# Optimization experiments

Measured on AMD Instinct MI355X. Metric: run time of the kernel, lower is better.

The kernel has to match this reference:

```python
import jax, jax.numpy as jnp
import numpy as np
from jax import lax


def _conv1d(z, w):
    # z: [B, C_in, L], w: [C_out, C_in, K], stride 1, padding 1 -> [B, C_out, L]
    return lax.conv_general_dilated(
        z, w, window_strides=(1,), padding=[(1, 1)],
        dimension_numbers=("NCH", "OIH", "NCH"))


def setup_inputs() -> dict:
    key = jax.random.key(0)
    k1, k2, k3 = jax.random.split(key, 3)
    B, T, C, H, L, K = 16, 64, 128, 256, 128, 3
    x = jax.random.normal(k1, (B, T, C, L), dtype=jnp.float32)
    # small init so tanh stays in its useful range
    W_i = jax.random.normal(k2, (H, C, K), dtype=jnp.float32) * 0.05
    W_h = jax.random.normal(k3, (H, H, K), dtype=jnp.float32) * 0.05
    return {"x": x, "W_i": W_i, "W_h": W_h}


def reference(x, W_i, W_h):
    # Conv1DRnn, single layer, unidirectional, no bias, mode RNN_TANH:
    #   h_t = tanh(conv_i(x_t) + conv_h(h_{t-1}))
    # x: [B, T, C, L] -> out: [B, T, H, L]
    B, T, C, L = x.shape
    H = W_i.shape[0]
    h0 = jnp.zeros((B, H, L), dtype=x.dtype)
    xt = jnp.swapaxes(x, 0, 1)  # [T, B, C, L]

    def step(h, x_t):
        h_new = jnp.tanh(_conv1d(x_t, W_i) + _conv1d(h, W_h))
        return h_new, h_new

    _, hs = lax.scan(step, h0, xt)  # hs: [T, B, H, L]
    return jnp.swapaxes(hs, 0, 1)   # [B, T, H, L]
```

## Files before the change

### kernel.cpp

```cpp
#include <hip/hip_runtime.h>
#include <math.h>

typedef _Float16 f16;
typedef _Float16 f16x2 __attribute__((ext_vector_type(2)));
typedef _Float16 f16x8 __attribute__((ext_vector_type(8)));
typedef float f32x4 __attribute__((ext_vector_type(4)));

#define LDIM 128
#define HOUT 256

__device__ __forceinline__ float tanh_fast(float x) {
    float a = fabsf(x);
    float e = __expf(-2.0f * a);
    float r = (1.0f - e) / (1.0f + e);
    return copysignf(r, x);
}

__device__ __forceinline__ void  st_agent(float* p, float v) {
    __hip_atomic_store(p, v, __ATOMIC_RELAXED, __HIP_MEMORY_SCOPE_AGENT);
}
__device__ __forceinline__ float ld_agent(const float* p) {
    return __hip_atomic_load(p, __ATOMIC_RELAXED, __HIP_MEMORY_SCOPE_AGENT);
}

__global__ void prep_w(const float* __restrict__ wi, f16* __restrict__ wti,
                       const float* __restrict__ wh, f16* __restrict__ wt2h)
{
    int idx = blockIdx.x * 256 + threadIdx.x;
    const int ni = 3 * HOUT * 128;
    if (idx < ni) {
        int k = idx / (HOUT * 128);
        int r = idx - k * (HOUT * 128);
        int h = r >> 7, c = r & 127;
        wti[idx] = (f16)wi[(h * 128 + c) * 3 + k];
    } else {
        int e = idx - ni;
        if (e >= 3 * HOUT * 256) return;
        int j    = e & 7;
        int lane = (e >> 3) & 63;
        int h16  = (e >> 9) & 15;
        int kk   = (e >> 13) & 7;
        int s    = e >> 16;
        int hh = h16 * 16 + (lane & 15);
        int c  = kk * 32 + (lane >> 4) * 8 + j;
        wt2h[e] = (f16)wh[(hh * 256 + c) * 3 + s];
    }
}

__global__ __launch_bounds__(256, 4)
void conv_i_all(const float* __restrict__ x, const f16* __restrict__ wt,
                float* __restrict__ out)
{
    __shared__ __align__(16) char smem[33792];
    const int tid = threadIdx.x;
    const int lane = tid & 63, wid = tid >> 6;
    const int wh = wid >> 1, wl = wid & 1;
    const int n   = blockIdx.x & 1023;
    const int sub = blockIdx.x >> 10;
    const int h0  = (sub >> 1) * 64;
    const int Lb  = (sub & 1) * 64;
    const int l16 = lane & 15, g = lane >> 4;

    const float* actn = x + (long)n * (128 * LDIM);

    {
        const int c4 = tid >> 4;
        const int rb = tid & 15;
        const int lg = Lb + rb * 4;
        f32x4 v[8];
#pragma unroll
        for (int ci = 0; ci < 8; ++ci)
            v[ci] = *(const f32x4*)(actn + (c4 * 8 + ci) * LDIM + lg);
#pragma unroll
        for (int i = 0; i < 4; ++i) {
            int r = rb * 4 + i + 1;
            f16x8 hi, lo;
#pragma unroll
            for (int ci = 0; ci < 8; ++ci) {
                float xx = v[ci][i];
                f16 h = (f16)xx;
                hi[ci] = h;
                lo[ci] = (f16)(xx - (float)h);
            }
            int base = r * 256 + ((c4 ^ (r & 7)) << 4);
            *(f16x8*)(smem + base) = hi;
            *(f16x8*)(smem + 16896 + base) = lo;
        }
        int cl = tid & 127, e = tid >> 7;
        int r = e ? 65 : 0;
        int lg2 = Lb + r - 1;
        float xx = ((unsigned)lg2 < 128u) ? actn[cl * LDIM + lg2] : 0.f;
        f16 h = (f16)xx;
        f16 lo = (f16)(xx - (float)h);
        int off = r * 256 + ((((cl >> 3) ^ (r & 7)) << 4)) + (cl & 7) * 2;
        *(f16*)(smem + off) = h;
        *(f16*)(smem + 16896 + off) = lo;
    }
    __syncthreads();

    f32x4 acc[2][2] = {};
#pragma unroll
    for (int kk = 0; kk < 4; ++kk) {
        f16x8 afr[3][2];
#pragma unroll
        for (int s = 0; s < 3; ++s)
#pragma unroll
            for (int hf = 0; hf < 2; ++hf) {
                int hh = h0 + wh * 32 + hf * 16 + l16;
                afr[s][hf] = *(const f16x8*)(wt + ((s * HOUT + hh) << 7) + kk * 32 + g * 8);
            }
#pragma unroll
        for (int s = 0; s < 3; ++s) {
            f16x8 bfr[2][2];
#pragma unroll
            for (int lf = 0; lf < 2; ++lf) {
                int r = wl * 32 + lf * 16 + l16 + s;
                int base = r * 256 + ((((kk * 4 + g) ^ (r & 7)) << 4));
                bfr[lf][0] = *(const f16x8*)(smem + base);
                bfr[lf][1] = *(const f16x8*)(smem + 16896 + base);
            }
#pragma unroll
            for (int hf = 0; hf < 2; ++hf)
#pragma unroll
                for (int lf = 0; lf < 2; ++lf) {
                    acc[hf][lf] = __builtin_amdgcn_mfma_f32_16x16x32_f16(
                        afr[s][hf], bfr[lf][0], acc[hf][lf], 0, 0, 0);
                    acc[hf][lf] = __builtin_amdgcn_mfma_f32_16x16x32_f16(
                        afr[s][hf], bfr[lf][1], acc[hf][lf], 0, 0, 0);
                }
        }
    }

    float* outn = out + (long)n * (HOUT * LDIM);
#pragma unroll
    for (int hf = 0; hf < 2; ++hf)
#pragma unroll
        for (int lf = 0; lf < 2; ++lf)
#pragma unroll
            for (int vv = 0; vv < 4; ++vv) {
                int hh = h0 + wh * 32 + hf * 16 + g * 4 + vv;
                int ll = Lb + wl * 32 + lf * 16 + l16;
                outn[hh * LDIM + ll] = acc[hf][lf][vv];
            }
}

__global__ __launch_bounds__(512, 2)
void rnn_persist(const f16* __restrict__ wt2, float* __restrict__ out,
                 unsigned* __restrict__ flags)
{
    __shared__ __align__(16) char smem[36864];
    const int tid  = threadIdx.x;
    const int lane = tid & 63, wid = tid >> 6;
    const int b    = blockIdx.x & 15;
    const int lw   = blockIdx.x >> 4;
    const int l0   = lw * 16;
    const int l16  = lane & 15, g = lane >> 4;
    const long HL  = (long)HOUT * LDIM;
    float* outb    = out + (long)b * (64 * HL);

    int deplw = lw;
    if (lane == 0 && lw > 0) deplw = lw - 1;
    if (lane == 1 && lw < 7) deplw = lw + 1;
    const unsigned* depflag = &flags[(b * 8 + deplw) * 16];
    unsigned* myflag = &flags[(b * 8 + lw) * 16];

    f16x8 afr[3][8][2];
#pragma unroll
    for (int s = 0; s < 3; ++s)
#pragma unroll
        for (int kk = 0; kk < 8; ++kk)
#pragma unroll
            for (int hf = 0; hf < 2; ++hf) {
                int h16 = wid * 2 + hf;
                afr[s][kk][hf] = *(const f16x8*)(wt2 +
                    ((((s * 8 + kk) * 16 + h16) * 64 + lane) << 3));
            }

    for (int t = 0; t < 64; ++t) {
        float* outt = outb + (long)t * HL;

        float z[2][4];
#pragma unroll
        for (int hf = 0; hf < 2; ++hf)
#pragma unroll
            for (int vv = 0; vv < 4; ++vv) {
                int c = wid * 32 + hf * 16 + g * 4 + vv;
                z[hf][vv] = outt[(long)c * LDIM + l0 + l16];
            }

        f32x4 acc[2] = {};
        if (t > 0) {
            const float* prev = outt - HL;

            {
                unsigned v = (lane < 2)
                    ? __hip_atomic_load(depflag, __ATOMIC_RELAXED, __HIP_MEMORY_SCOPE_AGENT)
                    : 0xFFFFFFFFu;
                while (__any(v < (unsigned)t)) {
                    __builtin_amdgcn_s_sleep(1);
                    if (lane < 2)
                        v = __hip_atomic_load(depflag, __ATOMIC_RELAXED, __HIP_MEMORY_SCOPE_AGENT);
                }
            }
            asm volatile("" ::: "memory");

            char* pr = smem + ((t - 1) & 1) * 18432;
            if (tid < 256) {
                int c = tid;
                float xx = (lw > 0) ? ld_agent(&prev[(long)c * LDIM + l0 - 1]) : 0.f;
                f16 h = (f16)xx, lo = (f16)(xx - (float)h);
                int off = ((c >> 3) << 4) + (c & 7) * 2;
                *(f16*)(pr + off) = h;
                *(f16*)(pr + 9216 + off) = lo;
            } else {
                int c = tid - 256;
                float xx = (lw < 7) ? ld_agent(&prev[(long)c * LDIM + l0 + 16]) : 0.f;
                f16 h = (f16)xx, lo = (f16)(xx - (float)h);
                int off = 17 * 512 + ((((c >> 3) ^ 1) << 4)) + (c & 7) * 2;
                *(f16*)(pr + off) = h;
                *(f16*)(pr + 9216 + off) = lo;
            }
            __syncthreads();

#pragma unroll
            for (int kk = 0; kk < 8; ++kk)
#pragma unroll
                for (int s = 0; s < 3; ++s) {
                    int r = l16 + s;
                    int base = r * 512 + ((((kk * 4 + g) ^ (r & 7)) << 4));
                    f16x8 b0 = *(const f16x8*)(pr + base);
                    f16x8 b1 = *(const f16x8*)(pr + 9216 + base);
#pragma unroll
                    for (int hf = 0; hf < 2; ++hf) {
                        acc[hf] = __builtin_amdgcn_mfma_f32_16x16x32_f16(
                            afr[s][kk][hf], b0, acc[hf], 0, 0, 0);
                        acc[hf] = __builtin_amdgcn_mfma_f32_16x16x32_f16(
                            afr[s][kk][hf], b1, acc[hf], 0, 0, 0);
                    }
                }
        }

        char* pw = smem + (t & 1) * 18432;
        const int r  = l16 + 1;
        const int rx = r & 7;
#pragma unroll
        for (int hf = 0; hf < 2; ++hf) {
            float hv[4];
#pragma unroll
            for (int vv = 0; vv < 4; ++vv) {
                int c = wid * 32 + hf * 16 + g * 4 + vv;
                hv[vv] = tanh_fast(acc[hf][vv] + z[hf][vv]);
                st_agent(&outt[(long)c * LDIM + l0 + l16], hv[vv]);
            }
#pragma unroll
            for (int p = 0; p < 2; ++p) {
                int c = wid * 32 + hf * 16 + g * 4 + p * 2;
                float a0 = hv[2 * p], a1 = hv[2 * p + 1];
                f16 h0 = (f16)a0, h1 = (f16)a1;
                f16 e0 = (f16)(a0 - (float)h0), e1 = (f16)(a1 - (float)h1);
                int off = r * 512 + ((((c >> 3) ^ rx) << 4)) + (c & 7) * 2;
                f16x2 hw; hw[0] = h0; hw[1] = h1;
                f16x2 ew; ew[0] = e0; ew[1] = e1;
                *(f16x2*)(pw + off) = hw;
                *(f16x2*)(pw + 9216 + off) = ew;
            }
        }
        __syncthreads();
        if (tid == 0)
            __hip_atomic_store(myflag, (unsigned)(t + 1),
                               __ATOMIC_RELAXED, __HIP_MEMORY_SCOPE_AGENT);
    }
}

extern "C" void kernel_launch(void* const* d_in, const int* in_sizes, int n_in,
                              void* d_out, int out_size, void* d_ws, size_t ws_size,
                              hipStream_t stream)
{
    const float* x   = (const float*)d_in[0];
    const float* W_i = (const float*)d_in[1];
    const float* W_h = (const float*)d_in[2];
    float* out = (float*)d_out;

    f16* wt_i  = (f16*)d_ws;
    f16* wt2_h = (f16*)((char*)d_ws + 196608);
    unsigned* flags = (unsigned*)((char*)d_ws + 589824);

    prep_w<<<1152, 256, 0, stream>>>(W_i, wt_i, W_h, wt2_h);
    hipMemsetAsync(flags, 0, 8192, stream);

    conv_i_all<<<8192, 256, 0, stream>>>(x, wt_i, out);
    rnn_persist<<<128, 512, 0, stream>>>(wt2_h, out, flags);
}
```

Measured before the change: 403.9 us.

## Fuse input convolution into persistent RNN kernel with tagged mailbox halo exchange

Drops the separate conv_i_all kernel. The persistent recurrent kernel now stages x for step t+2 and computes the input convolution for step t+1 while it waits on the current step's dependencies. Halo exchange between neighbouring blocks moves from a per-block flag plus a global reload of the previous h to 64-bit mailbox entries that pair a step tag with the value, and only the s=1 tap of the hidden convolution runs before the halo wait. This removes the out round trip for the input projection and a kernel launch, and shortens the critical-path sync. In exchange it adds input-conv work inside the serial loop and lowers occupancy to one block per CU.

```diff
diff --git a/kernel.cpp b/kernel.cpp
--- a/kernel.cpp
+++ b/kernel.cpp
@@ -5,9 +5,12 @@
 typedef _Float16 f16x2 __attribute__((ext_vector_type(2)));
 typedef _Float16 f16x8 __attribute__((ext_vector_type(8)));
 typedef float f32x4 __attribute__((ext_vector_type(4)));
+typedef unsigned long long u64;
 
 #define LDIM 128
 #define HOUT 256
+
+#define XB0 36864
 
 __device__ __forceinline__ float tanh_fast(float x) {
     float a = fabsf(x);
@@ -16,139 +19,120 @@
     return copysignf(r, x);
 }
 
-__device__ __forceinline__ void  st_agent(float* p, float v) {
+__device__ __forceinline__ void st_agent(float* p, float v) {
     __hip_atomic_store(p, v, __ATOMIC_RELAXED, __HIP_MEMORY_SCOPE_AGENT);
 }
-__device__ __forceinline__ float ld_agent(const float* p) {
+__device__ __forceinline__ void st_mb(u64* p, u64 v) {
+    __hip_atomic_store(p, v, __ATOMIC_RELAXED, __HIP_MEMORY_SCOPE_AGENT);
+}
+__device__ __forceinline__ u64 ld_mb(const u64* p) {
     return __hip_atomic_load(p, __ATOMIC_RELAXED, __HIP_MEMORY_SCOPE_AGENT);
 }
 
-__global__ void prep_w(const float* __restrict__ wi, f16* __restrict__ wti,
-                       const float* __restrict__ wh, f16* __restrict__ wt2h)
+__global__ void prep_w(const float* __restrict__ wi, f16* __restrict__ wtif,
+                       const float* __restrict__ wh, f16* __restrict__ wthf)
 {
     int idx = blockIdx.x * 256 + threadIdx.x;
-    const int ni = 3 * HOUT * 128;
+    const int ni = 3 * 4 * 16 * 64 * 8;
     if (idx < ni) {
-        int k = idx / (HOUT * 128);
-        int r = idx - k * (HOUT * 128);
-        int h = r >> 7, c = r & 127;
-        wti[idx] = (f16)wi[(h * 128 + c) * 3 + k];
+        int j    = idx & 7;
+        int lane = (idx >> 3) & 63;
+        int h16  = (idx >> 9) & 15;
+        int kk   = (idx >> 13) & 3;
+        int s    = idx >> 15;
+        int h = h16 * 16 + (lane & 15);
+        int c = kk * 32 + (lane >> 4) * 8 + j;
+        wtif[idx] = (f16)wi[(h * 128 + c) * 3 + s];
     } else {
         int e = idx - ni;
-        if (e >= 3 * HOUT * 256) return;
+        if (e >= 3 * 8 * 16 * 64 * 8) return;
         int j    = e & 7;
         int lane = (e >> 3) & 63;
         int h16  = (e >> 9) & 15;
         int kk   = (e >> 13) & 7;
         int s    = e >> 16;
-        int hh = h16 * 16 + (lane & 15);
-        int c  = kk * 32 + (lane >> 4) * 8 + j;
-        wt2h[e] = (f16)wh[(hh * 256 + c) * 3 + s];
-    }
-}
-
-__global__ __launch_bounds__(256, 4)
-void conv_i_all(const float* __restrict__ x, const f16* __restrict__ wt,
-                float* __restrict__ out)
-{
-    __shared__ __align__(16) char smem[33792];
-    const int tid = threadIdx.x;
-    const int lane = tid & 63, wid = tid >> 6;
-    const int wh = wid >> 1, wl = wid & 1;
-    const int n   = blockIdx.x & 1023;
-    const int sub = blockIdx.x >> 10;
-    const int h0  = (sub >> 1) * 64;
-    const int Lb  = (sub & 1) * 64;
-    const int l16 = lane & 15, g = lane >> 4;
-
-    const float* actn = x + (long)n * (128 * LDIM);
-
-    {
-        const int c4 = tid >> 4;
-        const int rb = tid & 15;
-        const int lg = Lb + rb * 4;
-        f32x4 v[8];
-#pragma unroll
-        for (int ci = 0; ci < 8; ++ci)
-            v[ci] = *(const f32x4*)(actn + (c4 * 8 + ci) * LDIM + lg);
-#pragma unroll
-        for (int i = 0; i < 4; ++i) {
-            int r = rb * 4 + i + 1;
-            f16x8 hi, lo;
-#pragma unroll
-            for (int ci = 0; ci < 8; ++ci) {
-                float xx = v[ci][i];
-                f16 h = (f16)xx;
-                hi[ci] = h;
-                lo[ci] = (f16)(xx - (float)h);
-            }
-            int base = r * 256 + ((c4 ^ (r & 7)) << 4);
-            *(f16x8*)(smem + base) = hi;
-            *(f16x8*)(smem + 16896 + base) = lo;
-        }
-        int cl = tid & 127, e = tid >> 7;
-        int r = e ? 65 : 0;
-        int lg2 = Lb + r - 1;
-        float xx = ((unsigned)lg2 < 128u) ? actn[cl * LDIM + lg2] : 0.f;
-        f16 h = (f16)xx;
-        f16 lo = (f16)(xx - (float)h);
-        int off = r * 256 + ((((cl >> 3) ^ (r & 7)) << 4)) + (cl & 7) * 2;
-        *(f16*)(smem + off) = h;
-        *(f16*)(smem + 16896 + off) = lo;
-    }
-    __syncthreads();
-
-    f32x4 acc[2][2] = {};
+        int h = h16 * 16 + (lane & 15);
+        int c = kk * 32 + (lane >> 4) * 8 + j;
+        wthf[e] = (f16)wh[(h * 256 + c) * 3 + s];
+    }
+}
+
+__device__ __forceinline__ void stage_x(char* xp, const float* __restrict__ xt,
+                                        int l0, int tid)
+{
+    const int c = tid >> 2, q = tid & 3;
+    f32x4 v = *(const f32x4*)(xt + c * LDIM + l0 + q * 4);
+#pragma unroll
+    for (int i = 0; i < 4; ++i) {
+        int r = q * 4 + i + 1;
+        float xx = v[i];
+        f16 h = (f16)xx, lo = (f16)(xx - (float)h);
+        int off = r * 256 + ((((c >> 3) ^ (r & 7)) << 4)) + (c & 7) * 2;
+        *(f16*)(xp + off) = h;
+        *(f16*)(xp + 4608 + off) = lo;
+    }
+    if (tid < 256) {
+        int e = tid >> 7, cc = tid & 127;
+        int l = e ? l0 + 16 : l0 - 1;
+        int r = e ? 17 : 0;
+        float xx = ((unsigned)l < 128u) ? xt[cc * LDIM + l] : 0.f;
+        f16 h = (f16)xx, lo = (f16)(xx - (float)h);
+        int off = r * 256 + ((((cc >> 3) ^ (r & 7)) << 4)) + (cc & 7) * 2;
+        *(f16*)(xp + off) = h;
+        *(f16*)(xp + 4608 + off) = lo;
+    }
+}
+
+__device__ __forceinline__ void zconv(const char* xp, const f16* __restrict__ wti,
+                                      int wid, int lane, int l16, int g, f32x4 zn[2])
+{
 #pragma unroll
     for (int kk = 0; kk < 4; ++kk) {
-        f16x8 afr[3][2];
+        f16x8 ai[3][2];
 #pragma unroll
         for (int s = 0; s < 3; ++s)
 #pragma unroll
+            for (int hf = 0; hf < 2; ++hf)
+                ai[s][hf] = *(const f16x8*)(wti +
+                    ((((s * 4 + kk) * 16 + wid * 2 + hf) * 64 + lane) << 3));
+#pragma unroll
+        for (int s = 0; s < 3; ++s) {
+            int r = l16 + s;
+            int base = r * 256 + ((((kk * 4 + g) ^ (r & 7)) << 4));
+            f16x8 b0 = *(const f16x8*)(xp + base);
+            f16x8 b1 = *(const f16x8*)(xp + 4608 + base);
+#pragma unroll
             for (int hf = 0; hf < 2; ++hf) {
-                int hh = h0 + wh * 32 + hf * 16 + l16;
-                afr[s][hf] = *(const f16x8*)(wt + ((s * HOUT + hh) << 7) + kk * 32 + g * 8);
-            }
-#pragma unroll
-        for (int s = 0; s < 3; ++s) {
-            f16x8 bfr[2][2];
-#pragma unroll
-            for (int lf = 0; lf < 2; ++lf) {
-                int r = wl * 32 + lf * 16 + l16 + s;
-                int base = r * 256 + ((((kk * 4 + g) ^ (r & 7)) << 4));
-                bfr[lf][0] = *(const f16x8*)(smem + base);
-                bfr[lf][1] = *(const f16x8*)(smem + 16896 + base);
-            }
-#pragma unroll
-            for (int hf = 0; hf < 2; ++hf)
-#pragma unroll
-                for (int lf = 0; lf < 2; ++lf) {
-                    acc[hf][lf] = __builtin_amdgcn_mfma_f32_16x16x32_f16(
-                        afr[s][hf], bfr[lf][0], acc[hf][lf], 0, 0, 0);
-                    acc[hf][lf] = __builtin_amdgcn_mfma_f32_16x16x32_f16(
-                        afr[s][hf], bfr[lf][1], acc[hf][lf], 0, 0, 0);
-                }
-        }
-    }
-
-    float* outn = out + (long)n * (HOUT * LDIM);
-#pragma unroll
-    for (int hf = 0; hf < 2; ++hf)
-#pragma unroll
-        for (int lf = 0; lf < 2; ++lf)
-#pragma unroll
-            for (int vv = 0; vv < 4; ++vv) {
-                int hh = h0 + wh * 32 + hf * 16 + g * 4 + vv;
-                int ll = Lb + wl * 32 + lf * 16 + l16;
-                outn[hh * LDIM + ll] = acc[hf][lf][vv];
-            }
-}
-
-__global__ __launch_bounds__(512, 2)
-void rnn_persist(const f16* __restrict__ wt2, float* __restrict__ out,
-                 unsigned* __restrict__ flags)
-{
-    __shared__ __align__(16) char smem[36864];
+                zn[hf] = __builtin_amdgcn_mfma_f32_16x16x32_f16(ai[s][hf], b0, zn[hf], 0, 0, 0);
+                zn[hf] = __builtin_amdgcn_mfma_f32_16x16x32_f16(ai[s][hf], b1, zn[hf], 0, 0, 0);
+            }
+        }
+    }
+}
+
+__device__ __forceinline__ void hconv_s(const char* hp, const f16x8 (*afr)[2],
+                                        int l16, int g, int s, f32x4 hacc[2])
+{
+#pragma unroll
+    for (int kk = 0; kk < 8; ++kk) {
+        int r = l16 + s;
+        int base = r * 512 + ((((kk * 4 + g) ^ (r & 7)) << 4));
+        f16x8 b0 = *(const f16x8*)(hp + base);
+        f16x8 b1 = *(const f16x8*)(hp + 9216 + base);
+#pragma unroll
+        for (int hf = 0; hf < 2; ++hf) {
+            hacc[hf] = __builtin_amdgcn_mfma_f32_16x16x32_f16(afr[kk][hf], b0, hacc[hf], 0, 0, 0);
+            hacc[hf] = __builtin_amdgcn_mfma_f32_16x16x32_f16(afr[kk][hf], b1, hacc[hf], 0, 0, 0);
+        }
+    }
+}
+
+__global__ __launch_bounds__(512, 1)
+void rnn_fused(const float* __restrict__ x, const f16* __restrict__ wti,
+               const f16* __restrict__ wth, float* __restrict__ out,
+               u64* __restrict__ mbox)
+{
+    __shared__ __align__(16) char smem[55296];
     const int tid  = threadIdx.x;
     const int lane = tid & 63, wid = tid >> 6;
     const int b    = blockIdx.x & 15;
@@ -157,100 +141,103 @@
     const int l16  = lane & 15, g = lane >> 4;
     const long HL  = (long)HOUT * LDIM;
     float* outb    = out + (long)b * (64 * HL);
-
-    int deplw = lw;
-    if (lane == 0 && lw > 0) deplw = lw - 1;
-    if (lane == 1 && lw < 7) deplw = lw + 1;
-    const unsigned* depflag = &flags[(b * 8 + deplw) * 16];
-    unsigned* myflag = &flags[(b * 8 + lw) * 16];
-
-    f16x8 afr[3][8][2];
+    const float* xb = x + (long)b * (64L * 128 * LDIM);
+
+    int edge = -1;
+    if (l16 == 0  && lw > 0) edge = 0;
+    if (l16 == 15 && lw < 7) edge = 1;
+    u64* mb_pub = (edge >= 0) ? (mbox + (((b * 8 + lw) * 2 + edge) * 2) * 256) : nullptr;
+
+    f16x8 afrh[3][8][2];
 #pragma unroll
     for (int s = 0; s < 3; ++s)
 #pragma unroll
         for (int kk = 0; kk < 8; ++kk)
 #pragma unroll
-            for (int hf = 0; hf < 2; ++hf) {
-                int h16 = wid * 2 + hf;
-                afr[s][kk][hf] = *(const f16x8*)(wt2 +
-                    ((((s * 8 + kk) * 16 + h16) * 64 + lane) << 3));
-            }
+            for (int hf = 0; hf < 2; ++hf)
+                afrh[s][kk][hf] = *(const f16x8*)(wth +
+                    ((((s * 8 + kk) * 16 + wid * 2 + hf) * 64 + lane) << 3));
+
+    stage_x(smem + XB0, xb, l0, tid);
+    stage_x(smem + XB0 + 9216, xb + 128 * LDIM, l0, tid);
+    __syncthreads();
+    f32x4 zcur[2] = {};
+    zconv(smem + XB0, wti, wid, lane, l16, g, zcur);
+    __syncthreads();
 
     for (int t = 0; t < 64; ++t) {
         float* outt = outb + (long)t * HL;
 
-        float z[2][4];
-#pragma unroll
-        for (int hf = 0; hf < 2; ++hf)
+        if (t + 2 < 64)
+            stage_x(smem + XB0 + (t & 1) * 9216, xb + (long)(t + 2) * (128 * LDIM), l0, tid);
+
+        f32x4 zn[2] = {};
+        if (t < 63)
+            zconv(smem + XB0 + ((t + 1) & 1) * 9216, wti, wid, lane, l16, g, zn);
+
+        f32x4 hacc[2] = {};
+        char* hp = smem + ((t ^ 1) & 1) * 18432;
+        if (t > 0)
+            hconv_s(hp, afrh[1], l16, g, 1, hacc);
+
+        if (t > 0) {
+            const int par = (t ^ 1) & 1;
+            if (tid < 256) {
+                int c = tid;
+                float xx = 0.f;
+                if (lw > 0) {
+                    const u64* p = mbox + ((((b * 8 + lw - 1) * 2 + 1) * 2 + par) * 256) + c;
+                    u64 v = ld_mb(p);
+                    while ((unsigned)(v >> 32) < (unsigned)t) {
+                        __builtin_amdgcn_s_sleep(1);
+                        v = ld_mb(p);
+                    }
+                    xx = __uint_as_float((unsigned)v);
+                }
+                f16 h = (f16)xx, lo = (f16)(xx - (float)h);
+                int off = ((c >> 3) << 4) + (c & 7) * 2;
+                *(f16*)(hp + off) = h;
+                *(f16*)(hp + 9216 + off) = lo;
+            } else {
+                int c = tid - 256;
+                float xx = 0.f;
+                if (lw < 7) {
+                    const u64* p = mbox + ((((b * 8 + lw + 1) * 2 + 0) * 2 + par) * 256) + c;
+                    u64 v = ld_mb(p);
+                    while ((unsigned)(v >> 32) < (unsigned)t) {
+                        __builtin_amdgcn_s_sleep(1);
+                        v = ld_mb(p);
+                    }
+                    xx = __uint_as_float((unsigned)v);
+                }
+                f16 h = (f16)xx, lo = (f16)(xx - (float)h);
+                int off = 17 * 512 + ((((c >> 3) ^ 1) << 4)) + (c & 7) * 2;
+                *(f16*)(hp + off) = h;
+                *(f16*)(hp + 9216 + off) = lo;
+            }
+        }
+        __syncthreads();
+
+        if (t > 0) {
+            hconv_s(hp, afrh[0], l16, g, 0, hacc);
+            hconv_s(hp, afrh[2], l16, g, 2, hacc);
+        }
+
+        char* pw = smem + (t & 1) * 18432;
+        u64* pub = (edge >= 0) ? (mb_pub + (t & 1) * 256) : nullptr;
+        const u64 tagw = ((u64)(unsigned)(t + 1)) << 32;
+        const int r  = l16 + 1;
+        const int rx = r & 7;
+#pragma unroll
+        for (int hf = 0; hf < 2; ++hf) {
+            float hv[4];
 #pragma unroll
             for (int vv = 0; vv < 4; ++vv) {
                 int c = wid * 32 + hf * 16 + g * 4 + vv;
-                z[hf][vv] = outt[(long)c * LDIM + l0 + l16];
-            }
-
-        f32x4 acc[2] = {};
-        if (t > 0) {
-            const float* prev = outt - HL;
-
-            {
-                unsigned v = (lane < 2)
-                    ? __hip_atomic_load(depflag, __ATOMIC_RELAXED, __HIP_MEMORY_SCOPE_AGENT)
-                    : 0xFFFFFFFFu;
-                while (__any(v < (unsigned)t)) {
-                    __builtin_amdgcn_s_sleep(1);
-                    if (lane < 2)
-                        v = __hip_atomic_load(depflag, __ATOMIC_RELAXED, __HIP_MEMORY_SCOPE_AGENT);
-                }
-            }
-            asm volatile("" ::: "memory");
-
-            char* pr = smem + ((t - 1) & 1) * 18432;
-            if (tid < 256) {
-                int c = tid;
-                float xx = (lw > 0) ? ld_agent(&prev[(long)c * LDIM + l0 - 1]) : 0.f;
-                f16 h = (f16)xx, lo = (f16)(xx - (float)h);
-                int off = ((c >> 3) << 4) + (c & 7) * 2;
-                *(f16*)(pr + off) = h;
-                *(f16*)(pr + 9216 + off) = lo;
-            } else {
-                int c = tid - 256;
-                float xx = (lw < 7) ? ld_agent(&prev[(long)c * LDIM + l0 + 16]) : 0.f;
-                f16 h = (f16)xx, lo = (f16)(xx - (float)h);
-                int off = 17 * 512 + ((((c >> 3) ^ 1) << 4)) + (c & 7) * 2;
-                *(f16*)(pr + off) = h;
-                *(f16*)(pr + 9216 + off) = lo;
-            }
-            __syncthreads();
-
-#pragma unroll
-            for (int kk = 0; kk < 8; ++kk)
-#pragma unroll
-                for (int s = 0; s < 3; ++s) {
-                    int r = l16 + s;
-                    int base = r * 512 + ((((kk * 4 + g) ^ (r & 7)) << 4));
-                    f16x8 b0 = *(const f16x8*)(pr + base);
-                    f16x8 b1 = *(const f16x8*)(pr + 9216 + base);
-#pragma unroll
-                    for (int hf = 0; hf < 2; ++hf) {
-                        acc[hf] = __builtin_amdgcn_mfma_f32_16x16x32_f16(
-                            afr[s][kk][hf], b0, acc[hf], 0, 0, 0);
-                        acc[hf] = __builtin_amdgcn_mfma_f32_16x16x32_f16(
-                            afr[s][kk][hf], b1, acc[hf], 0, 0, 0);
-                    }
-                }
-        }
-
-        char* pw = smem + (t & 1) * 18432;
-        const int r  = l16 + 1;
-        const int rx = r & 7;
-#pragma unroll
-        for (int hf = 0; hf < 2; ++hf) {
-            float hv[4];
-#pragma unroll
-            for (int vv = 0; vv < 4; ++vv) {
-                int c = wid * 32 + hf * 16 + g * 4 + vv;
-                hv[vv] = tanh_fast(acc[hf][vv] + z[hf][vv]);
+                hv[vv] = tanh_fast(hacc[hf][vv] + zcur[hf][vv]);
                 st_agent(&outt[(long)c * LDIM + l0 + l16], hv[vv]);
+                if (edge >= 0)
+                    st_mb(&pub[c], tagw | (u64)__float_as_uint(hv[vv]));
             }
 #pragma unroll
             for (int p = 0; p < 2; ++p) {
@@ -265,10 +252,10 @@
                 *(f16x2*)(pw + 9216 + off) = ew;
             }
         }
+        zcur[0] = zn[0];
+        zcur[1] = zn[1];
+
         __syncthreads();
-        if (tid == 0)
-            __hip_atomic_store(myflag, (unsigned)(t + 1),
-                               __ATOMIC_RELAXED, __HIP_MEMORY_SCOPE_AGENT);
     }
 }
 
@@ -281,13 +268,12 @@
     const float* W_h = (const float*)d_in[2];
     float* out = (float*)d_out;
 
-    f16* wt_i  = (f16*)d_ws;
-    f16* wt2_h = (f16*)((char*)d_ws + 196608);
-    unsigned* flags = (unsigned*)((char*)d_ws + 589824);
-
-    prep_w<<<1152, 256, 0, stream>>>(W_i, wt_i, W_h, wt2_h);
-    hipMemsetAsync(flags, 0, 8192, stream);
-
-    conv_i_all<<<8192, 256, 0, stream>>>(x, wt_i, out);
-    rnn_persist<<<128, 512, 0, stream>>>(wt2_h, out, flags);
-}
+    f16* wt_i = (f16*)d_ws;
+    f16* wt_h = (f16*)((char*)d_ws + 196608);
+    u64* mbox = (u64*)((char*)d_ws + 589824);
+
+    prep_w<<<1152, 256, 0, stream>>>(W_i, wt_i, W_h, wt_h);
+    hipMemsetAsync(mbox, 0, 131072, stream);
+
+    rnn_fused<<<128, 512, 0, stream>>>(x, wt_i, wt_h, out, mbox);
+}
```

Result: slower. 1.020 ms (+152.5%).
